# Optimization experiments

Measured on AMD Instinct MI355X. Metric: run time of the kernel, lower is better.

## Reference

```python
import jax, jax.numpy as jnp
import numpy as np

RADIUS = 5            # min(max(5, ceil(80/20)), 80) = 5
SPATIAL_SIGMA = 4.0
INTENSITY_SIGMA = 1.0
EPS_MEAN = 1e-5
EPS_DEN = 1e-6


def gaussian_kernel(radius, sigma, dtype):
    # norm.pdf(d/sigma)/norm.pdf(0) == exp(-d^2 / (2*sigma^2))
    x2 = jnp.arange(-radius, radius + 1, dtype=dtype) ** 2
    d2 = x2[:, None, None] + x2[None, :, None] + x2[None, None, :]
    k = jnp.exp(-d2 / (2.0 * sigma * sigma))
    return k[None, None]  # OIDHW: [1,1,2r+1,2r+1,2r+1]


def conv3d_same(x, kernel):
    # x: [B,1,H,W,D]; 'same' padding with radius on all spatial dims
    pad = [(RADIUS, RADIUS)] * 3
    return jax.lax.conv_general_dilated(
        x, kernel, window_strides=(1, 1, 1), padding=pad,
        dimension_numbers=('NCDHW', 'OIDHW', 'NCDHW'))


def setup_inputs() -> dict:
    key = jax.random.key(0)
    k1, k2 = jax.random.split(key)
    labels = jax.random.uniform(k1, (2, 4, 80, 80, 80), dtype=jnp.float32)
    inputs = jax.random.uniform(k2, (2, 1, 80, 80, 80), dtype=jnp.float32)
    return {"labels": labels, "inputs": inputs}


def reference(labels, inputs):
    N, K, H, W, D = labels.shape
    kernel = gaussian_kernel(RADIUS, SPATIAL_SIGMA, labels.dtype)

    probs = labels[:, :, None]          # [N,K,1,H,W,D]
    img = inputs[:, None]               # [N,1,C,H,W,D]

    # per-class mean intensity: [N,K,C,1,1,1]
    class_mean = (jnp.mean(img * probs, axis=(3, 4, 5), keepdims=True)
                  / (jnp.mean(probs, axis=(3, 4, 5), keepdims=True) + EPS_MEAN))
    diff = jnp.sum((img - class_mean) ** 2, axis=2)        # [N,K,H,W,D]
    weights = jnp.exp(-(diff ** 2) / (INTENSITY_SIGMA ** 2))  # [N,K,H,W,D]

    # batch the K independent single-channel 3D convs as [N*K,1,H,W,D]
    pw = (labels * weights).reshape(N * K, 1, H, W, D)
    w = weights.reshape(N * K, 1, H, W, D)
    conv_pw = conv3d_same(pw, kernel).reshape(N, K, H, W, D)
    conv_w = conv3d_same(w, kernel).reshape(N, K, H, W, D)

    numerator = jnp.sum(labels * conv_pw, axis=(2, 3, 4))   # [N,K]
    denominator = jnp.sum(labels * conv_w, axis=(2, 3, 4))  # [N,K]
    ratio = numerator / (denominator + EPS_DEN)

    # torch L1Loss(num/den, 0) = mean over batch N, summed over classes k
    loss = jnp.sum(jnp.mean(jnp.abs(ratio), axis=0))
    return K - loss
```

## Files before the change

### kernel.cpp

```cpp
#include <hip/hip_runtime.h>
#include <math.h>

#define RAD 5
#define SIDE 80
#define SLAB 6400
#define VOL 512000
#define NCH 8
#define NCLS 4
#define TW 16
#define NT 5
#define NBLK1 (NCH*SIDE*NT)
#define Q 20
#define TBS 22
#define NBLK2 1000
#define CPB 125

__constant__ float GW[11] = {
    0.45783336177161427f, 0.6065306597126334f, 0.7548396019890073f,
    0.8824969025845955f,  0.969233234476344f,  1.0f,
    0.969233234476344f,   0.8824969025845955f, 0.7548396019890073f,
    0.6065306597126334f,  0.45783336177161427f};

__device__ float  g_bufT[(size_t)NCH * VOL];
__device__ float2 g_part1[NBLK1];
__device__ float2 g_part2[NBLK2];

__global__ void __launch_bounds__(256) convdw_sums_kernel(
        const float* __restrict__ labels, const float* __restrict__ img) {
    const int tile = blockIdx.x;
    const int c   = tile / (SIDE * NT);
    const int rem = tile % (SIDE * NT);
    const int h   = rem / NT;
    const int w0  = (rem % NT) * TW;
    const int n   = c >> 2;

    __shared__ float4 tB[26 * TBS];
    __shared__ float sm[8];

    const float4* labc4 = (const float4*)(labels + ((size_t)c * SIDE + h) * SLAB);
    const float4* imgc4 = (const float4*)(img + ((size_t)n * SIDE + h) * SLAB);

    float sip = 0.f, sp = 0.f;
    for (int i = threadIdx.x; i < 26 * Q; i += 256) {
        const int r = i / Q, q = i - (i / Q) * Q;
        const int w = w0 - RAD + r;
        float a[20];
        #pragma unroll
        for (int j = 0; j < 20; ++j) a[j] = 0.f;
        if (w >= 0 && w < SIDE) {
            const float4* row = labc4 + (size_t)w * Q;
            #pragma unroll
            for (int j = 0; j < 5; ++j) {
                int qq = q - 2 + j;
                if (qq >= 0 && qq < Q) {
                    float4 v = row[qq];
                    a[4 * j] = v.x; a[4 * j + 1] = v.y;
                    a[4 * j + 2] = v.z; a[4 * j + 3] = v.w;
                }
            }
            if (r >= RAD && r < RAD + TW) {
                float4 v = imgc4[(size_t)w * Q + q];
                sip += a[8] * v.x + a[9] * v.y + a[10] * v.z + a[11] * v.w;
                sp  += a[8] + a[9] + a[10] + a[11];
            }
        }
        float s0 = 0.f, s1 = 0.f, s2 = 0.f, s3 = 0.f;
        #pragma unroll
        for (int t = 0; t < 11; ++t) {
            float g = GW[t];
            s0 += g * a[t + 3]; s1 += g * a[t + 4];
            s2 += g * a[t + 5]; s3 += g * a[t + 6];
        }
        tB[r * TBS + q] = make_float4(s0, s1, s2, s3);
    }
    #pragma unroll
    for (int off = 32; off > 0; off >>= 1) {
        sip += __shfl_down(sip, off);
        sp  += __shfl_down(sp, off);
    }
    const int lane = threadIdx.x & 63;
    const int wid  = threadIdx.x >> 6;
    if (lane == 0) { sm[wid * 2] = sip; sm[wid * 2 + 1] = sp; }
    __syncthreads();
    if (threadIdx.x == 0)
        g_part1[tile] = make_float2(sm[0] + sm[2] + sm[4] + sm[6],
                                    sm[1] + sm[3] + sm[5] + sm[7]);
    float* outc = g_bufT + (size_t)c * VOL + (size_t)h * SIDE;
    for (int i = threadIdx.x; i < TW * Q; i += 256) {
        const int rl = i / Q, q = i - (i / Q) * Q;
        float sx = 0.f, sy = 0.f, sz = 0.f, sw = 0.f;
        #pragma unroll
        for (int t = 0; t < 11; ++t) {
            float g = GW[t];
            float4 v = tB[(rl + t) * TBS + q];
            sx += g * v.x; sy += g * v.y; sz += g * v.z; sw += g * v.w;
        }
        ((float4*)(outc + (size_t)(w0 + rl) * SLAB))[q] = make_float4(sx, sy, sz, sw);
    }
}

__global__ void __launch_bounds__(256) convh_dot_kernel(
        const float* __restrict__ labels, const float* __restrict__ img) {
    const int c = blockIdx.x / CPB;
    const int tid = blockIdx.x * 256 + threadIdx.x;
    const int rem = tid % (CPB * 256);
    const int hq  = rem / 1600;
    const int r2  = rem % 1600;
    const int w   = r2 / Q;
    const int q   = r2 % Q;
    const int h0  = hq * 4;
    const int n   = c >> 2;

    __shared__ float sm[8];
    __shared__ float s_mean;

    float a = 0.f, b = 0.f;
    for (int t = threadIdx.x; t < SIDE * NT; t += 256) {
        float2 p = g_part1[c * (SIDE * NT) + t];
        a += p.x; b += p.y;
    }
    #pragma unroll
    for (int off = 32; off > 0; off >>= 1) {
        a += __shfl_down(a, off);
        b += __shfl_down(b, off);
    }
    const int lane = threadIdx.x & 63;
    const int wid  = threadIdx.x >> 6;
    if (lane == 0) { sm[wid * 2] = a; sm[wid * 2 + 1] = b; }
    __syncthreads();
    if (threadIdx.x == 0)
        s_mean = (sm[0] + sm[2] + sm[4] + sm[6]) /
                 (sm[1] + sm[3] + sm[5] + sm[7] + 5.12f);
    __syncthreads();
    const float mean = s_mean;

    const float4* bc4 = (const float4*)g_bufT + (size_t)c * (VOL / 4) + (size_t)w * (SLAB / 4);
    float4 win[14];
    #pragma unroll
    for (int m = 0; m < 14; ++m) {
        int hh = h0 - RAD + m;
        win[m] = (hh >= 0 && hh < SIDE) ? bc4[hh * Q + q]
                                        : make_float4(0.f, 0.f, 0.f, 0.f);
    }
    const float4* labp4 = (const float4*)labels + (size_t)c * (VOL / 4);
    const float4* imgp4 = (const float4*)img + (size_t)n * (VOL / 4);
    float num = 0.f, den = 0.f;
    #pragma unroll
    for (int k = 0; k < 4; ++k) {
        float sx = 0.f, sy = 0.f, sz = 0.f, sw = 0.f;
        #pragma unroll
        for (int t = 0; t < 11; ++t) {
            float g = GW[t];
            float4 v = win[k + t];
            sx += g * v.x; sy += g * v.y; sz += g * v.z; sw += g * v.w;
        }
        size_t gi = (size_t)(h0 + k) * (SLAB / 4) + (size_t)w * Q + q;
        float4 l = labp4[gi];
        float4 v = imgp4[gi];
        float d0 = v.x - mean, d1 = v.y - mean, d2 = v.z - mean, d3 = v.w - mean;
        float q0 = d0 * d0, q1 = d1 * d1, q2 = d2 * d2, q3 = d3 * d3;
        float w0_ = __expf(-q0 * q0), w1_ = __expf(-q1 * q1);
        float w2_ = __expf(-q2 * q2), w3_ = __expf(-q3 * q3);
        num += sx * l.x * w0_ + sy * l.y * w1_ + sz * l.z * w2_ + sw * l.w * w3_;
        den += sx * w0_ + sy * w1_ + sz * w2_ + sw * w3_;
    }
    #pragma unroll
    for (int off = 32; off > 0; off >>= 1) {
        num += __shfl_down(num, off);
        den += __shfl_down(den, off);
    }
    if (lane == 0) { sm[wid * 2] = num; sm[wid * 2 + 1] = den; }
    __syncthreads();
    if (threadIdx.x == 0)
        g_part2[blockIdx.x] = make_float2(sm[0] + sm[2] + sm[4] + sm[6],
                                          sm[1] + sm[3] + sm[5] + sm[7]);
}

__global__ void __launch_bounds__(256) final_kernel(float* __restrict__ out) {
    __shared__ float sm[8];
    __shared__ float cn[NCH], cd[NCH];
    const int lane = threadIdx.x & 63;
    const int wid  = threadIdx.x >> 6;
    for (int c = 0; c < NCH; ++c) {
        float a = 0.f, b = 0.f;
        for (int t = threadIdx.x; t < CPB; t += 256) {
            float2 p = g_part2[c * CPB + t];
            a += p.x; b += p.y;
        }
        #pragma unroll
        for (int off = 32; off > 0; off >>= 1) {
            a += __shfl_down(a, off);
            b += __shfl_down(b, off);
        }
        if (lane == 0) { sm[wid * 2] = a; sm[wid * 2 + 1] = b; }
        __syncthreads();
        if (threadIdx.x == 0) {
            cn[c] = sm[0] + sm[2] + sm[4] + sm[6];
            cd[c] = sm[1] + sm[3] + sm[5] + sm[7];
        }
        __syncthreads();
    }
    if (threadIdx.x == 0) {
        float loss = 0.f;
        for (int k = 0; k < NCLS; ++k) {
            float r0 = cn[k]        / (cd[k]        + 1e-6f);
            float r1 = cn[NCLS + k] / (cd[NCLS + k] + 1e-6f);
            loss += 0.5f * (fabsf(r0) + fabsf(r1));
        }
        out[0] = (float)NCLS - loss;
    }
}

extern "C" void kernel_launch(void* const* d_in, const int* in_sizes, int n_in,
                              void* d_out, int out_size, void* d_ws, size_t ws_size,
                              hipStream_t stream) {
    const float* labels = (const float*)d_in[0];
    const float* img    = (const float*)d_in[1];
    float* out = (float*)d_out;
    (void)d_ws; (void)ws_size;

    hipLaunchKernelGGL(convdw_sums_kernel, dim3(NBLK1), dim3(256), 0, stream, labels, img);
    hipLaunchKernelGGL(convh_dot_kernel,   dim3(NBLK2), dim3(256), 0, stream, labels, img);
    hipLaunchKernelGGL(final_kernel,       dim3(1),     dim3(256), 0, stream, out);
}
```

Before: 98.21 us.

## Fuse separable 3D conv into one streaming kernel with register-held H pass

The old version wrote the D/W-convolved volume to a global intermediate buffer and read it back in a second kernel for the H pass and dot product. The new version splits out the per-class sums into a small reduction kernel. A single tiled kernel then streams H rows through shared memory, doing the D and W passes in LDS and accumulating the H pass in an 11-entry register ring, fused with the weighted dot. This removes the 16 MB intermediate round-trip through global memory. In exchange it launches only 200 blocks of 320 threads, which may underfill the GPU, and it has a long serial loop of 26 steps with two syncs per step.

```diff
diff --git a/kernel.cpp b/kernel.cpp
--- a/kernel.cpp
+++ b/kernel.cpp
@@ -7,13 +7,16 @@
 #define VOL 512000
 #define NCH 8
 #define NCLS 4
+#define Q 20
+#define TH 16
 #define TW 16
-#define NT 5
-#define NBLK1 (NCH*SIDE*NT)
-#define Q 20
-#define TBS 22
-#define NBLK2 1000
-#define CPB 125
+#define NTH 5
+#define NTW 5
+#define TPC (NTH*NTW)
+#define NBLK1 (NCH*TPC)
+#define SUMB 64
+#define ROWS 24
+#define VS 21
 
 __constant__ float GW[11] = {
     0.45783336177161427f, 0.6065306597126334f, 0.7548396019890073f,
@@ -21,187 +24,173 @@
     0.969233234476344f,   0.8824969025845955f, 0.7548396019890073f,
     0.6065306597126334f,  0.45783336177161427f};
 
-__device__ float  g_bufT[(size_t)NCH * VOL];
-__device__ float2 g_part1[NBLK1];
-__device__ float2 g_part2[NBLK2];
-
-__global__ void __launch_bounds__(256) convdw_sums_kernel(
+__device__ float2 g_s1[NCH * SUMB];
+__device__ float2 g_part[NBLK1];
+
+__global__ void __launch_bounds__(256) sums_kernel(
         const float* __restrict__ labels, const float* __restrict__ img) {
-    const int tile = blockIdx.x;
-    const int c   = tile / (SIDE * NT);
-    const int rem = tile % (SIDE * NT);
-    const int h   = rem / NT;
-    const int w0  = (rem % NT) * TW;
-    const int n   = c >> 2;
-
-    __shared__ float4 tB[26 * TBS];
-    __shared__ float sm[8];
-
-    const float4* labc4 = (const float4*)(labels + ((size_t)c * SIDE + h) * SLAB);
-    const float4* imgc4 = (const float4*)(img + ((size_t)n * SIDE + h) * SLAB);
-
+    const int c = blockIdx.y;
+    const int n = c >> 2;
+    const float4* lab4 = (const float4*)labels + (size_t)c * (VOL / 4);
+    const float4* img4 = (const float4*)img + (size_t)n * (VOL / 4);
     float sip = 0.f, sp = 0.f;
-    for (int i = threadIdx.x; i < 26 * Q; i += 256) {
-        const int r = i / Q, q = i - (i / Q) * Q;
-        const int w = w0 - RAD + r;
-        float a[20];
-        #pragma unroll
-        for (int j = 0; j < 20; ++j) a[j] = 0.f;
-        if (w >= 0 && w < SIDE) {
-            const float4* row = labc4 + (size_t)w * Q;
-            #pragma unroll
-            for (int j = 0; j < 5; ++j) {
-                int qq = q - 2 + j;
-                if (qq >= 0 && qq < Q) {
-                    float4 v = row[qq];
-                    a[4 * j] = v.x; a[4 * j + 1] = v.y;
-                    a[4 * j + 2] = v.z; a[4 * j + 3] = v.w;
-                }
-            }
-            if (r >= RAD && r < RAD + TW) {
-                float4 v = imgc4[(size_t)w * Q + q];
-                sip += a[8] * v.x + a[9] * v.y + a[10] * v.z + a[11] * v.w;
-                sp  += a[8] + a[9] + a[10] + a[11];
-            }
-        }
-        float s0 = 0.f, s1 = 0.f, s2 = 0.f, s3 = 0.f;
-        #pragma unroll
-        for (int t = 0; t < 11; ++t) {
-            float g = GW[t];
-            s0 += g * a[t + 3]; s1 += g * a[t + 4];
-            s2 += g * a[t + 5]; s3 += g * a[t + 6];
-        }
-        tB[r * TBS + q] = make_float4(s0, s1, s2, s3);
+    for (int i = blockIdx.x * 256 + threadIdx.x; i < VOL / 4; i += SUMB * 256) {
+        float4 l = lab4[i];
+        float4 v = img4[i];
+        sip += l.x * v.x + l.y * v.y + l.z * v.z + l.w * v.w;
+        sp  += l.x + l.y + l.z + l.w;
     }
     #pragma unroll
     for (int off = 32; off > 0; off >>= 1) {
         sip += __shfl_down(sip, off);
         sp  += __shfl_down(sp, off);
     }
+    __shared__ float sm[8];
     const int lane = threadIdx.x & 63;
     const int wid  = threadIdx.x >> 6;
     if (lane == 0) { sm[wid * 2] = sip; sm[wid * 2 + 1] = sp; }
     __syncthreads();
     if (threadIdx.x == 0)
-        g_part1[tile] = make_float2(sm[0] + sm[2] + sm[4] + sm[6],
-                                    sm[1] + sm[3] + sm[5] + sm[7]);
-    float* outc = g_bufT + (size_t)c * VOL + (size_t)h * SIDE;
-    for (int i = threadIdx.x; i < TW * Q; i += 256) {
-        const int rl = i / Q, q = i - (i / Q) * Q;
-        float sx = 0.f, sy = 0.f, sz = 0.f, sw = 0.f;
+        g_s1[c * SUMB + blockIdx.x] = make_float2(sm[0] + sm[2] + sm[4] + sm[6],
+                                                  sm[1] + sm[3] + sm[5] + sm[7]);
+}
+
+__global__ void __launch_bounds__(320) conv_dot_kernel(
+        const float* __restrict__ labels, const float* __restrict__ img) {
+    const int blk = blockIdx.x;
+    const int c   = blk / TPC;
+    const int r   = blk % TPC;
+    const int h0  = (r / NTW) * TH;
+    const int w0  = (r % NTW) * TW;
+    const int n   = c >> 2;
+    const int tid = threadIdx.x;
+    const int w_l = tid / Q;
+    const int q   = tid % Q;
+
+    __shared__ float4 rowb[2][26 * ROWS];
+    __shared__ float4 Vb[2][26 * VS];
+    __shared__ float sm[10];
+    __shared__ float s_mean;
+
+    if (tid < 64) {
+        float2 p = g_s1[c * SUMB + tid];
+        float a = p.x, b = p.y;
+        #pragma unroll
+        for (int off = 32; off > 0; off >>= 1) {
+            a += __shfl_down(a, off);
+            b += __shfl_down(b, off);
+        }
+        if (tid == 0) s_mean = a / (b + 5.12f);
+    }
+    for (int i = tid; i < 2 * 26 * 4; i += 320) {
+        int b = i / 104, rr = (i % 104) >> 2, j = i & 3;
+        rowb[b][rr * ROWS + ((j < 2) ? j : (20 + j))] = make_float4(0.f, 0.f, 0.f, 0.f);
+    }
+    __syncthreads();
+    const float mean = s_mean;
+
+    const float4* labc4 = (const float4*)labels + (size_t)c * (VOL / 4);
+    const float4* imgc4 = (const float4*)img + (size_t)n * (VOL / 4);
+
+    float4 P[11];
+    #pragma unroll
+    for (int k = 0; k < 11; ++k) P[k] = make_float4(0.f, 0.f, 0.f, 0.f);
+    float num = 0.f, den = 0.f;
+
+    #pragma unroll 2
+    for (int it = 0; it < 26; ++it) {
+        const int p = it & 1;
+        const int h = h0 - RAD + it;
+        const bool hv = (unsigned)h < SIDE;
+        for (int s = tid; s < 26 * Q; s += 320) {
+            int ws = s / Q, qs = s - (s / Q) * Q;
+            int w = w0 - RAD + ws;
+            float4 v = make_float4(0.f, 0.f, 0.f, 0.f);
+            if (hv && (unsigned)w < SIDE)
+                v = labc4[((size_t)h * SIDE + w) * Q + qs];
+            rowb[p][ws * ROWS + 2 + qs] = v;
+        }
+        __syncthreads();
+        for (int s = tid; s < 26 * Q; s += 320) {
+            int ws = s / Q, qs = s - (s / Q) * Q;
+            float a[20];
+            #pragma unroll
+            for (int j = 0; j < 5; ++j) {
+                float4 v = rowb[p][ws * ROWS + qs + j];
+                a[4 * j] = v.x; a[4 * j + 1] = v.y;
+                a[4 * j + 2] = v.z; a[4 * j + 3] = v.w;
+            }
+            float s0 = 0.f, s1 = 0.f, s2 = 0.f, s3 = 0.f;
+            #pragma unroll
+            for (int t = 0; t < 11; ++t) {
+                float g = GW[t];
+                s0 += g * a[t + 3]; s1 += g * a[t + 4];
+                s2 += g * a[t + 5]; s3 += g * a[t + 6];
+            }
+            Vb[p][ws * VS + qs] = make_float4(s0, s1, s2, s3);
+        }
+        __syncthreads();
+        float4 U = make_float4(0.f, 0.f, 0.f, 0.f);
         #pragma unroll
         for (int t = 0; t < 11; ++t) {
             float g = GW[t];
-            float4 v = tB[(rl + t) * TBS + q];
-            sx += g * v.x; sy += g * v.y; sz += g * v.z; sw += g * v.w;
-        }
-        ((float4*)(outc + (size_t)(w0 + rl) * SLAB))[q] = make_float4(sx, sy, sz, sw);
-    }
-}
-
-__global__ void __launch_bounds__(256) convh_dot_kernel(
-        const float* __restrict__ labels, const float* __restrict__ img) {
-    const int c = blockIdx.x / CPB;
-    const int tid = blockIdx.x * 256 + threadIdx.x;
-    const int rem = tid % (CPB * 256);
-    const int hq  = rem / 1600;
-    const int r2  = rem % 1600;
-    const int w   = r2 / Q;
-    const int q   = r2 % Q;
-    const int h0  = hq * 4;
-    const int n   = c >> 2;
-
-    __shared__ float sm[8];
-    __shared__ float s_mean;
-
-    float a = 0.f, b = 0.f;
-    for (int t = threadIdx.x; t < SIDE * NT; t += 256) {
-        float2 p = g_part1[c * (SIDE * NT) + t];
-        a += p.x; b += p.y;
-    }
-    #pragma unroll
-    for (int off = 32; off > 0; off >>= 1) {
-        a += __shfl_down(a, off);
-        b += __shfl_down(b, off);
-    }
-    const int lane = threadIdx.x & 63;
-    const int wid  = threadIdx.x >> 6;
-    if (lane == 0) { sm[wid * 2] = a; sm[wid * 2 + 1] = b; }
-    __syncthreads();
-    if (threadIdx.x == 0)
-        s_mean = (sm[0] + sm[2] + sm[4] + sm[6]) /
-                 (sm[1] + sm[3] + sm[5] + sm[7] + 5.12f);
-    __syncthreads();
-    const float mean = s_mean;
-
-    const float4* bc4 = (const float4*)g_bufT + (size_t)c * (VOL / 4) + (size_t)w * (SLAB / 4);
-    float4 win[14];
-    #pragma unroll
-    for (int m = 0; m < 14; ++m) {
-        int hh = h0 - RAD + m;
-        win[m] = (hh >= 0 && hh < SIDE) ? bc4[hh * Q + q]
-                                        : make_float4(0.f, 0.f, 0.f, 0.f);
-    }
-    const float4* labp4 = (const float4*)labels + (size_t)c * (VOL / 4);
-    const float4* imgp4 = (const float4*)img + (size_t)n * (VOL / 4);
-    float num = 0.f, den = 0.f;
-    #pragma unroll
-    for (int k = 0; k < 4; ++k) {
-        float sx = 0.f, sy = 0.f, sz = 0.f, sw = 0.f;
-        #pragma unroll
-        for (int t = 0; t < 11; ++t) {
-            float g = GW[t];
-            float4 v = win[k + t];
-            sx += g * v.x; sy += g * v.y; sz += g * v.z; sw += g * v.w;
-        }
-        size_t gi = (size_t)(h0 + k) * (SLAB / 4) + (size_t)w * Q + q;
-        float4 l = labp4[gi];
-        float4 v = imgp4[gi];
-        float d0 = v.x - mean, d1 = v.y - mean, d2 = v.z - mean, d3 = v.w - mean;
-        float q0 = d0 * d0, q1 = d1 * d1, q2 = d2 * d2, q3 = d3 * d3;
-        float w0_ = __expf(-q0 * q0), w1_ = __expf(-q1 * q1);
-        float w2_ = __expf(-q2 * q2), w3_ = __expf(-q3 * q3);
-        num += sx * l.x * w0_ + sy * l.y * w1_ + sz * l.z * w2_ + sw * l.w * w3_;
-        den += sx * w0_ + sy * w1_ + sz * w2_ + sw * w3_;
+            float4 v = Vb[p][(w_l + t) * VS + q];
+            U.x += g * v.x; U.y += g * v.y; U.z += g * v.z; U.w += g * v.w;
+        }
+        #pragma unroll
+        for (int k = 0; k < 11; ++k) {
+            float g = GW[k];
+            P[k].x += g * U.x; P[k].y += g * U.y;
+            P[k].z += g * U.z; P[k].w += g * U.w;
+        }
+        if (it >= 10) {
+            const int m = h0 + it - 10;
+            size_t gi = ((size_t)m * SIDE + (w0 + w_l)) * Q + q;
+            float4 l = labc4[gi];
+            float4 v = imgc4[gi];
+            float4 o = P[0];
+            float d0 = v.x - mean, d1 = v.y - mean, d2 = v.z - mean, d3 = v.w - mean;
+            float q0 = d0 * d0, q1 = d1 * d1, q2 = d2 * d2, q3 = d3 * d3;
+            float e0 = __expf(-q0 * q0), e1 = __expf(-q1 * q1);
+            float e2 = __expf(-q2 * q2), e3 = __expf(-q3 * q3);
+            num += o.x * l.x * e0 + o.y * l.y * e1 + o.z * l.z * e2 + o.w * l.w * e3;
+            den += o.x * e0 + o.y * e1 + o.z * e2 + o.w * e3;
+        }
+        #pragma unroll
+        for (int k = 0; k < 10; ++k) P[k] = P[k + 1];
+        P[10] = make_float4(0.f, 0.f, 0.f, 0.f);
     }
     #pragma unroll
     for (int off = 32; off > 0; off >>= 1) {
         num += __shfl_down(num, off);
         den += __shfl_down(den, off);
     }
+    const int lane = tid & 63;
+    const int wid  = tid >> 6;
     if (lane == 0) { sm[wid * 2] = num; sm[wid * 2 + 1] = den; }
     __syncthreads();
-    if (threadIdx.x == 0)
-        g_part2[blockIdx.x] = make_float2(sm[0] + sm[2] + sm[4] + sm[6],
-                                          sm[1] + sm[3] + sm[5] + sm[7]);
-}
-
-__global__ void __launch_bounds__(256) final_kernel(float* __restrict__ out) {
-    __shared__ float sm[8];
-    __shared__ float cn[NCH], cd[NCH];
-    const int lane = threadIdx.x & 63;
-    const int wid  = threadIdx.x >> 6;
+    if (tid == 0)
+        g_part[blk] = make_float2(sm[0] + sm[2] + sm[4] + sm[6] + sm[8],
+                                  sm[1] + sm[3] + sm[5] + sm[7] + sm[9]);
+}
+
+__global__ void __launch_bounds__(64) final_kernel(float* __restrict__ out) {
+    const int t = threadIdx.x;
+    float cn[NCH], cd[NCH];
+    #pragma unroll
     for (int c = 0; c < NCH; ++c) {
         float a = 0.f, b = 0.f;
-        for (int t = threadIdx.x; t < CPB; t += 256) {
-            float2 p = g_part2[c * CPB + t];
-            a += p.x; b += p.y;
-        }
+        if (t < TPC) { float2 p = g_part[c * TPC + t]; a = p.x; b = p.y; }
         #pragma unroll
         for (int off = 32; off > 0; off >>= 1) {
             a += __shfl_down(a, off);
             b += __shfl_down(b, off);
         }
-        if (lane == 0) { sm[wid * 2] = a; sm[wid * 2 + 1] = b; }
-        __syncthreads();
-        if (threadIdx.x == 0) {
-            cn[c] = sm[0] + sm[2] + sm[4] + sm[6];
-            cd[c] = sm[1] + sm[3] + sm[5] + sm[7];
-        }
-        __syncthreads();
-    }
-    if (threadIdx.x == 0) {
+        cn[c] = a; cd[c] = b;
+    }
+    if (t == 0) {
         float loss = 0.f;
+        #pragma unroll
         for (int k = 0; k < NCLS; ++k) {
             float r0 = cn[k]        / (cd[k]        + 1e-6f);
             float r1 = cn[NCLS + k] / (cd[NCLS + k] + 1e-6f);
@@ -219,7 +208,7 @@
     float* out = (float*)d_out;
     (void)d_ws; (void)ws_size;
 
-    hipLaunchKernelGGL(convdw_sums_kernel, dim3(NBLK1), dim3(256), 0, stream, labels, img);
-    hipLaunchKernelGGL(convh_dot_kernel,   dim3(NBLK2), dim3(256), 0, stream, labels, img);
-    hipLaunchKernelGGL(final_kernel,       dim3(1),     dim3(256), 0, stream, out);
-}
+    hipLaunchKernelGGL(sums_kernel,     dim3(SUMB, NCH), dim3(256), 0, stream, labels, img);
+    hipLaunchKernelGGL(conv_dot_kernel, dim3(NBLK1),     dim3(320), 0, stream, labels, img);
+    hipLaunchKernelGGL(final_kernel,    dim3(1),         dim3(64),  0, stream, out);
+}
```

Measured after the change: 126.1 us. 1.28x slower.

## Enlarge conv tiles to cut halo reloads and simplify final reduction

Applied to the files above, without the earlier changes.

Widens the w-tile of the first separable-conv kernel from 16 to 40 columns and doubles the h-rows each thread handles in the second kernel (18-entry sliding window, 320-thread blocks). This reduces redundant halo loads and recomputation in both conv passes. The final reduction now uses a single wavefront with shuffles instead of shared memory and barriers. The cost is fewer blocks, which lowers occupancy and latency hiding, and higher register pressure.

```diff
diff --git a/kernel.cpp b/kernel.cpp
--- a/kernel.cpp
+++ b/kernel.cpp
@@ -7,13 +7,18 @@
 #define VOL 512000
 #define NCH 8
 #define NCLS 4
-#define TW 16
-#define NT 5
-#define NBLK1 (NCH*SIDE*NT)
 #define Q 20
 #define TBS 22
-#define NBLK2 1000
-#define CPB 125
+
+#define WT 40
+#define K1ROWS 50
+#define NWT 2
+#define C1 (SIDE*NWT)
+#define NBLK1 (NCH*C1)
+
+#define K2T 320
+#define K2PB 50
+#define NBLK2 (NCH*K2PB)
 
 __constant__ float GW[11] = {
     0.45783336177161427f, 0.6065306597126334f, 0.7548396019890073f,
@@ -28,26 +33,27 @@
 __global__ void __launch_bounds__(256) convdw_sums_kernel(
         const float* __restrict__ labels, const float* __restrict__ img) {
     const int tile = blockIdx.x;
-    const int c   = tile / (SIDE * NT);
-    const int rem = tile % (SIDE * NT);
-    const int h   = rem / NT;
-    const int w0  = (rem % NT) * TW;
+    const int c   = tile / C1;
+    const int rem = tile % C1;
+    const int h   = rem / NWT;
+    const int w0  = (rem % NWT) * WT;
     const int n   = c >> 2;
 
-    __shared__ float4 tB[26 * TBS];
+    __shared__ float4 tB[K1ROWS * TBS];
     __shared__ float sm[8];
 
-    const float4* labc4 = (const float4*)(labels + ((size_t)c * SIDE + h) * SLAB);
+    const float4* labc4 = (const float4*)labels + ((size_t)c * SIDE + h) * Q * SIDE / 4 * 4 / (Q * 4) * 0;
+    labc4 = (const float4*)(labels + ((size_t)c * SIDE + h) * SLAB);
     const float4* imgc4 = (const float4*)(img + ((size_t)n * SIDE + h) * SLAB);
 
     float sip = 0.f, sp = 0.f;
-    for (int i = threadIdx.x; i < 26 * Q; i += 256) {
+    for (int i = threadIdx.x; i < K1ROWS * Q; i += 256) {
         const int r = i / Q, q = i - (i / Q) * Q;
         const int w = w0 - RAD + r;
         float a[20];
         #pragma unroll
         for (int j = 0; j < 20; ++j) a[j] = 0.f;
-        if (w >= 0 && w < SIDE) {
+        if ((unsigned)w < SIDE) {
             const float4* row = labc4 + (size_t)w * Q;
             #pragma unroll
             for (int j = 0; j < 5; ++j) {
@@ -58,7 +64,7 @@
                     a[4 * j + 2] = v.z; a[4 * j + 3] = v.w;
                 }
             }
-            if (r >= RAD && r < RAD + TW) {
+            if (r >= RAD && r < RAD + WT) {
                 float4 v = imgc4[(size_t)w * Q + q];
                 sip += a[8] * v.x + a[9] * v.y + a[10] * v.z + a[11] * v.w;
                 sp  += a[8] + a[9] + a[10] + a[11];
@@ -86,7 +92,7 @@
         g_part1[tile] = make_float2(sm[0] + sm[2] + sm[4] + sm[6],
                                     sm[1] + sm[3] + sm[5] + sm[7]);
     float* outc = g_bufT + (size_t)c * VOL + (size_t)h * SIDE;
-    for (int i = threadIdx.x; i < TW * Q; i += 256) {
+    for (int i = threadIdx.x; i < WT * Q; i += 256) {
         const int rl = i / Q, q = i - (i / Q) * Q;
         float sx = 0.f, sy = 0.f, sz = 0.f, sw = 0.f;
         #pragma unroll
@@ -99,24 +105,23 @@
     }
 }
 
-__global__ void __launch_bounds__(256) convh_dot_kernel(
+__global__ void __launch_bounds__(K2T) convh_dot_kernel(
         const float* __restrict__ labels, const float* __restrict__ img) {
-    const int c = blockIdx.x / CPB;
-    const int tid = blockIdx.x * 256 + threadIdx.x;
-    const int rem = tid % (CPB * 256);
+    const int c   = blockIdx.x / K2PB;
+    const int rem = (blockIdx.x % K2PB) * K2T + threadIdx.x;
     const int hq  = rem / 1600;
     const int r2  = rem % 1600;
     const int w   = r2 / Q;
     const int q   = r2 % Q;
-    const int h0  = hq * 4;
+    const int h0  = hq * 8;
     const int n   = c >> 2;
 
-    __shared__ float sm[8];
+    __shared__ float sm[10];
     __shared__ float s_mean;
 
     float a = 0.f, b = 0.f;
-    for (int t = threadIdx.x; t < SIDE * NT; t += 256) {
-        float2 p = g_part1[c * (SIDE * NT) + t];
+    for (int t = threadIdx.x; t < C1; t += K2T) {
+        float2 p = g_part1[c * C1 + t];
         a += p.x; b += p.y;
     }
     #pragma unroll
@@ -129,24 +134,24 @@
     if (lane == 0) { sm[wid * 2] = a; sm[wid * 2 + 1] = b; }
     __syncthreads();
     if (threadIdx.x == 0)
-        s_mean = (sm[0] + sm[2] + sm[4] + sm[6]) /
-                 (sm[1] + sm[3] + sm[5] + sm[7] + 5.12f);
+        s_mean = (sm[0] + sm[2] + sm[4] + sm[6] + sm[8]) /
+                 (sm[1] + sm[3] + sm[5] + sm[7] + sm[9] + 5.12f);
     __syncthreads();
     const float mean = s_mean;
 
     const float4* bc4 = (const float4*)g_bufT + (size_t)c * (VOL / 4) + (size_t)w * (SLAB / 4);
-    float4 win[14];
-    #pragma unroll
-    for (int m = 0; m < 14; ++m) {
+    float4 win[18];
+    #pragma unroll
+    for (int m = 0; m < 18; ++m) {
         int hh = h0 - RAD + m;
-        win[m] = (hh >= 0 && hh < SIDE) ? bc4[hh * Q + q]
-                                        : make_float4(0.f, 0.f, 0.f, 0.f);
+        win[m] = ((unsigned)hh < SIDE) ? bc4[hh * Q + q]
+                                       : make_float4(0.f, 0.f, 0.f, 0.f);
     }
     const float4* labp4 = (const float4*)labels + (size_t)c * (VOL / 4);
     const float4* imgp4 = (const float4*)img + (size_t)n * (VOL / 4);
     float num = 0.f, den = 0.f;
     #pragma unroll
-    for (int k = 0; k < 4; ++k) {
+    for (int k = 0; k < 8; ++k) {
         float sx = 0.f, sy = 0.f, sz = 0.f, sw = 0.f;
         #pragma unroll
         for (int t = 0; t < 11; ++t) {
@@ -159,10 +164,10 @@
         float4 v = imgp4[gi];
         float d0 = v.x - mean, d1 = v.y - mean, d2 = v.z - mean, d3 = v.w - mean;
         float q0 = d0 * d0, q1 = d1 * d1, q2 = d2 * d2, q3 = d3 * d3;
-        float w0_ = __expf(-q0 * q0), w1_ = __expf(-q1 * q1);
-        float w2_ = __expf(-q2 * q2), w3_ = __expf(-q3 * q3);
-        num += sx * l.x * w0_ + sy * l.y * w1_ + sz * l.z * w2_ + sw * l.w * w3_;
-        den += sx * w0_ + sy * w1_ + sz * w2_ + sw * w3_;
+        float e0 = __expf(-q0 * q0), e1 = __expf(-q1 * q1);
+        float e2 = __expf(-q2 * q2), e3 = __expf(-q3 * q3);
+        num += sx * l.x * e0 + sy * l.y * e1 + sz * l.z * e2 + sw * l.w * e3;
+        den += sx * e0 + sy * e1 + sz * e2 + sw * e3;
     }
     #pragma unroll
     for (int off = 32; off > 0; off >>= 1) {
@@ -172,36 +177,27 @@
     if (lane == 0) { sm[wid * 2] = num; sm[wid * 2 + 1] = den; }
     __syncthreads();
     if (threadIdx.x == 0)
-        g_part2[blockIdx.x] = make_float2(sm[0] + sm[2] + sm[4] + sm[6],
-                                          sm[1] + sm[3] + sm[5] + sm[7]);
-}
-
-__global__ void __launch_bounds__(256) final_kernel(float* __restrict__ out) {
-    __shared__ float sm[8];
-    __shared__ float cn[NCH], cd[NCH];
-    const int lane = threadIdx.x & 63;
-    const int wid  = threadIdx.x >> 6;
+        g_part2[blockIdx.x] = make_float2(sm[0] + sm[2] + sm[4] + sm[6] + sm[8],
+                                          sm[1] + sm[3] + sm[5] + sm[7] + sm[9]);
+}
+
+__global__ void __launch_bounds__(64) final_kernel(float* __restrict__ out) {
+    const int t = threadIdx.x;
+    float cn[NCH], cd[NCH];
+    #pragma unroll
     for (int c = 0; c < NCH; ++c) {
         float a = 0.f, b = 0.f;
-        for (int t = threadIdx.x; t < CPB; t += 256) {
-            float2 p = g_part2[c * CPB + t];
-            a += p.x; b += p.y;
-        }
+        if (t < K2PB) { float2 p = g_part2[c * K2PB + t]; a = p.x; b = p.y; }
         #pragma unroll
         for (int off = 32; off > 0; off >>= 1) {
             a += __shfl_down(a, off);
             b += __shfl_down(b, off);
         }
-        if (lane == 0) { sm[wid * 2] = a; sm[wid * 2 + 1] = b; }
-        __syncthreads();
-        if (threadIdx.x == 0) {
-            cn[c] = sm[0] + sm[2] + sm[4] + sm[6];
-            cd[c] = sm[1] + sm[3] + sm[5] + sm[7];
-        }
-        __syncthreads();
-    }
-    if (threadIdx.x == 0) {
+        cn[c] = a; cd[c] = b;
+    }
+    if (t == 0) {
         float loss = 0.f;
+        #pragma unroll
         for (int k = 0; k < NCLS; ++k) {
             float r0 = cn[k]        / (cd[k]        + 1e-6f);
             float r1 = cn[NCLS + k] / (cd[NCLS + k] + 1e-6f);
@@ -220,6 +216,6 @@
     (void)d_ws; (void)ws_size;
 
     hipLaunchKernelGGL(convdw_sums_kernel, dim3(NBLK1), dim3(256), 0, stream, labels, img);
-    hipLaunchKernelGGL(convh_dot_kernel,   dim3(NBLK2), dim3(256), 0, stream, labels, img);
-    hipLaunchKernelGGL(final_kernel,       dim3(1),     dim3(256), 0, stream, out);
-}
+    hipLaunchKernelGGL(convh_dot_kernel,   dim3(NBLK2), dim3(K2T), 0, stream, labels, img);
+    hipLaunchKernelGGL(final_kernel,       dim3(1),     dim3(64),  0, stream, out);
+}
```

New measurement: 102.5 us. 4.4% more time.

## Store intermediate separable-conv buffer in bf16 and halve rows per thread

Applied to the files above, without the earlier changes.

The D/W-convolved intermediate buffer is now stored as bf16 (round-to-nearest-even) instead of fp32, and converted back to float when loaded for the H-direction pass. This halves the bytes written by the first kernel and read by the second. The second kernel also computes 2 H rows per thread instead of 4, doubling the block count for more parallelism. In exchange each output needs more window loads (12 loads for 2 rows instead of 14 for 4), and bf16 rounding adds a small error to the convolution sums.

```diff
diff --git a/kernel.cpp b/kernel.cpp
--- a/kernel.cpp
+++ b/kernel.cpp
@@ -7,13 +7,14 @@
 #define VOL 512000
 #define NCH 8
 #define NCLS 4
+#define Q 20
 #define TW 16
 #define NT 5
-#define NBLK1 (NCH*SIDE*NT)
-#define Q 20
+#define C1 (SIDE*NT)
+#define NBLK1 (NCH*C1)
 #define TBS 22
-#define NBLK2 1000
-#define CPB 125
+#define K2PB 250
+#define NBLK2 (NCH*K2PB)
 
 __constant__ float GW[11] = {
     0.45783336177161427f, 0.6065306597126334f, 0.7548396019890073f,
@@ -21,15 +22,24 @@
     0.969233234476344f,   0.8824969025845955f, 0.7548396019890073f,
     0.6065306597126334f,  0.45783336177161427f};
 
-__device__ float  g_bufT[(size_t)NCH * VOL];
+__device__ unsigned short g_bufT[(size_t)NCH * VOL];
 __device__ float2 g_part1[NBLK1];
 __device__ float2 g_part2[NBLK2];
+
+__device__ __forceinline__ unsigned short f2bf(float f) {
+    unsigned u = __float_as_uint(f);
+    u += 0x7FFFu + ((u >> 16) & 1u);
+    return (unsigned short)(u >> 16);
+}
+__device__ __forceinline__ float bf2f(unsigned short h) {
+    return __uint_as_float((unsigned)h << 16);
+}
 
 __global__ void __launch_bounds__(256) convdw_sums_kernel(
         const float* __restrict__ labels, const float* __restrict__ img) {
     const int tile = blockIdx.x;
-    const int c   = tile / (SIDE * NT);
-    const int rem = tile % (SIDE * NT);
+    const int c   = tile / C1;
+    const int rem = tile % C1;
     const int h   = rem / NT;
     const int w0  = (rem % NT) * TW;
     const int n   = c >> 2;
@@ -47,7 +57,7 @@
         float a[20];
         #pragma unroll
         for (int j = 0; j < 20; ++j) a[j] = 0.f;
-        if (w >= 0 && w < SIDE) {
+        if ((unsigned)w < SIDE) {
             const float4* row = labc4 + (size_t)w * Q;
             #pragma unroll
             for (int j = 0; j < 5; ++j) {
@@ -85,7 +95,7 @@
     if (threadIdx.x == 0)
         g_part1[tile] = make_float2(sm[0] + sm[2] + sm[4] + sm[6],
                                     sm[1] + sm[3] + sm[5] + sm[7]);
-    float* outc = g_bufT + (size_t)c * VOL + (size_t)h * SIDE;
+    ushort4* out4 = (ushort4*)g_bufT + ((size_t)c * VOL + (size_t)h * SIDE) / 4;
     for (int i = threadIdx.x; i < TW * Q; i += 256) {
         const int rl = i / Q, q = i - (i / Q) * Q;
         float sx = 0.f, sy = 0.f, sz = 0.f, sw = 0.f;
@@ -95,28 +105,29 @@
             float4 v = tB[(rl + t) * TBS + q];
             sx += g * v.x; sy += g * v.y; sz += g * v.z; sw += g * v.w;
         }
-        ((float4*)(outc + (size_t)(w0 + rl) * SLAB))[q] = make_float4(sx, sy, sz, sw);
+        ushort4 o;
+        o.x = f2bf(sx); o.y = f2bf(sy); o.z = f2bf(sz); o.w = f2bf(sw);
+        out4[(size_t)(w0 + rl) * (SLAB / 4) + q] = o;
     }
 }
 
 __global__ void __launch_bounds__(256) convh_dot_kernel(
         const float* __restrict__ labels, const float* __restrict__ img) {
-    const int c = blockIdx.x / CPB;
-    const int tid = blockIdx.x * 256 + threadIdx.x;
-    const int rem = tid % (CPB * 256);
-    const int hq  = rem / 1600;
+    const int c   = blockIdx.x / K2PB;
+    const int rem = (blockIdx.x % K2PB) * 256 + threadIdx.x;
+    const int hp  = rem / 1600;
     const int r2  = rem % 1600;
     const int w   = r2 / Q;
     const int q   = r2 % Q;
-    const int h0  = hq * 4;
+    const int h0  = hp * 2;
     const int n   = c >> 2;
 
     __shared__ float sm[8];
     __shared__ float s_mean;
 
     float a = 0.f, b = 0.f;
-    for (int t = threadIdx.x; t < SIDE * NT; t += 256) {
-        float2 p = g_part1[c * (SIDE * NT) + t];
+    for (int t = threadIdx.x; t < C1; t += 256) {
+        float2 p = g_part1[c * C1 + t];
         a += p.x; b += p.y;
     }
     #pragma unroll
@@ -134,19 +145,23 @@
     __syncthreads();
     const float mean = s_mean;
 
-    const float4* bc4 = (const float4*)g_bufT + (size_t)c * (VOL / 4) + (size_t)w * (SLAB / 4);
-    float4 win[14];
-    #pragma unroll
-    for (int m = 0; m < 14; ++m) {
+    const ushort4* bc4 = (const ushort4*)g_bufT + ((size_t)c * VOL + (size_t)w * SLAB) / 4;
+    float4 win[12];
+    #pragma unroll
+    for (int m = 0; m < 12; ++m) {
         int hh = h0 - RAD + m;
-        win[m] = (hh >= 0 && hh < SIDE) ? bc4[hh * Q + q]
-                                        : make_float4(0.f, 0.f, 0.f, 0.f);
+        if ((unsigned)hh < SIDE) {
+            ushort4 u = bc4[hh * (SIDE / 4) + q];
+            win[m] = make_float4(bf2f(u.x), bf2f(u.y), bf2f(u.z), bf2f(u.w));
+        } else {
+            win[m] = make_float4(0.f, 0.f, 0.f, 0.f);
+        }
     }
     const float4* labp4 = (const float4*)labels + (size_t)c * (VOL / 4);
     const float4* imgp4 = (const float4*)img + (size_t)n * (VOL / 4);
     float num = 0.f, den = 0.f;
     #pragma unroll
-    for (int k = 0; k < 4; ++k) {
+    for (int k = 0; k < 2; ++k) {
         float sx = 0.f, sy = 0.f, sz = 0.f, sw = 0.f;
         #pragma unroll
         for (int t = 0; t < 11; ++t) {
@@ -159,10 +174,10 @@
         float4 v = imgp4[gi];
         float d0 = v.x - mean, d1 = v.y - mean, d2 = v.z - mean, d3 = v.w - mean;
         float q0 = d0 * d0, q1 = d1 * d1, q2 = d2 * d2, q3 = d3 * d3;
-        float w0_ = __expf(-q0 * q0), w1_ = __expf(-q1 * q1);
-        float w2_ = __expf(-q2 * q2), w3_ = __expf(-q3 * q3);
-        num += sx * l.x * w0_ + sy * l.y * w1_ + sz * l.z * w2_ + sw * l.w * w3_;
-        den += sx * w0_ + sy * w1_ + sz * w2_ + sw * w3_;
+        float e0 = __expf(-q0 * q0), e1 = __expf(-q1 * q1);
+        float e2 = __expf(-q2 * q2), e3 = __expf(-q3 * q3);
+        num += sx * l.x * e0 + sy * l.y * e1 + sz * l.z * e2 + sw * l.w * e3;
+        den += sx * e0 + sy * e1 + sz * e2 + sw * e3;
     }
     #pragma unroll
     for (int off = 32; off > 0; off >>= 1) {
@@ -183,8 +198,8 @@
     const int wid  = threadIdx.x >> 6;
     for (int c = 0; c < NCH; ++c) {
         float a = 0.f, b = 0.f;
-        for (int t = threadIdx.x; t < CPB; t += 256) {
-            float2 p = g_part2[c * CPB + t];
+        for (int t = threadIdx.x; t < K2PB; t += 256) {
+            float2 p = g_part2[c * K2PB + t];
             a += p.x; b += p.y;
         }
         #pragma unroll
```

Result: no change. 99.40 us (+1.2%).
